# Performance work log

Hardware: AMD Instinct MI355X
Metric: run time of the kernel (lower is better)

Reference implementation:

```python
import jax, jax.numpy as jnp
import numpy as np
from jax import lax

B, T, D, A = 32, 2048, 1024, 1024

def setup_inputs() -> dict:
    key = jax.random.key(0)
    ks = jax.random.split(key, 8)
    s = 1.0 / np.sqrt(D)
    return {
        "query": jax.random.normal(ks[0], (B, 1, D), jnp.float32),
        "value": jax.random.normal(ks[1], (B, T, D), jnp.float32),
        "last_attn": jax.random.uniform(ks[2], (B, T), jnp.float32),
        "conv_w": jax.random.normal(ks[3], (A, 1, 3), jnp.float32) * 0.1,
        "conv_b": jnp.zeros((A,), jnp.float32),
        "Wq": jax.random.normal(ks[4], (A, D), jnp.float32) * s,
        "Wv": jax.random.normal(ks[5], (A, D), jnp.float32) * s,
        "bias": jax.random.uniform(ks[6], (A,), jnp.float32, -0.1, 0.1),
        "fc_w": jax.random.normal(ks[7], (1, A), jnp.float32) * (1.0 / np.sqrt(A)),
        "fc_b": jnp.zeros((1,), jnp.float32),
    }

def reference(query, value, last_attn, conv_w, conv_b, Wq, Wv, bias, fc_w, fc_b):
    # location conv1d: (B,1,T) -> (B,A,T), kernel 3, pad 1
    loc = lax.conv_general_dilated(
        last_attn[:, None, :], conv_w, window_strides=(1,), padding="SAME",
        dimension_numbers=("NCH", "OIH", "NCH"))
    loc = loc + conv_b[None, :, None]
    loc = jnp.transpose(loc, (0, 2, 1))  # (B, T, A)
    # fused add + bias + tanh; query proj (B,1,A) broadcasts over T
    hidden = jnp.tanh(query @ Wq.T + value @ Wv.T + loc + bias)  # (B, T, A)
    energy = (hidden @ fc_w.T + fc_b)[..., 0]  # (B, T)
    attn = jax.nn.softmax(energy, axis=-1)  # (B, T)
    context = jnp.einsum("bt,btd->bd", attn, value)[:, None, :]  # (B, 1, D)
    return context, attn
```

## Files before the change

kernel.cpp:

```cpp
#include <hip/hip_runtime.h>
#include <stdint.h>

#define AS1 __attribute__((address_space(1)))
#define AS3 __attribute__((address_space(3)))

typedef __bf16 bf16x8 __attribute__((ext_vector_type(8)));
typedef float  f32x4  __attribute__((ext_vector_type(4)));

__global__ __launch_bounds__(256) void cast_bf16(const float* __restrict__ in,
                                                 __bf16* __restrict__ out, int n8) {
    int i = blockIdx.x * 256 + threadIdx.x;
    if (i >= n8) return;
    const float4* p = (const float4*)in + (size_t)i * 2;
    float4 x = p[0], y = p[1];
    bf16x8 v;
    v[0] = (__bf16)x.x; v[1] = (__bf16)x.y; v[2] = (__bf16)x.z; v[3] = (__bf16)x.w;
    v[4] = (__bf16)y.x; v[5] = (__bf16)y.y; v[6] = (__bf16)y.z; v[7] = (__bf16)y.w;
    *((bf16x8*)out + i) = v;
}

__global__ __launch_bounds__(256) void prep_qb2(const float* __restrict__ q,
                                                const float* __restrict__ Wq,
                                                const float* __restrict__ bias,
                                                const float* __restrict__ convb,
                                                float* __restrict__ qb2) {
    int wid  = threadIdx.x >> 6;
    int lane = threadIdx.x & 63;
    int a    = blockIdx.x * 4 + wid;
    const float* wr_ = Wq + (size_t)a * 1024;
    float w[16];
#pragma unroll
    for (int j = 0; j < 16; ++j) w[j] = wr_[lane + 64 * j];
    float bb = bias[a] + convb[a];
    for (int b = 0; b < 32; ++b) {
        const float* qr = q + (size_t)b * 1024;
        float s = 0.f;
#pragma unroll
        for (int j = 0; j < 16; ++j) s += w[j] * qr[lane + 64 * j];
        for (int m = 1; m < 64; m <<= 1) s += __shfl_xor(s, m);
        if (lane == 0) qb2[b * 1024 + a] = s + bb;
    }
}

__global__ __launch_bounds__(256, 4) void gemm_fused(
    const __bf16* __restrict__ Abf,
    const __bf16* __restrict__ Bbf,
    const float*  __restrict__ qb2,
    const float*  __restrict__ la,
    const float*  __restrict__ convw,
    const float*  __restrict__ fcw,
    float* __restrict__ ep)
{
    constexpr int K = 1024, NT = 16;
    __shared__ __bf16 As[128 * 64];
    __shared__ __bf16 Bs[128 * 64];

    const int tid  = threadIdx.x;
    const int lane = tid & 63;
    const int wid  = tid >> 6;
    const int wr   = wid >> 1, wc = wid & 1;

    const int bid = blockIdx.x;
    const int swz = (bid & 7) * 512 + (bid >> 3);
    const int rt  = swz >> 3;
    const int ct  = swz & 7;
    const int rowBase = rt * 128;
    const int colBase = ct * 128;

    f32x4 acc[4][4] = {};

#pragma unroll 1
    for (int t = 0; t < NT; ++t) {
        const int k0 = t * 64;
#pragma unroll
        for (int is = 0; is < 4; ++is) {
            int idx16 = is * 256 + tid;
            int r     = idx16 >> 3;
            int ssw   = (idx16 ^ r) & 7;
            const __bf16* ga = Abf + (size_t)(rowBase + r) * K + k0 + ssw * 8;
            __builtin_amdgcn_global_load_lds((AS1 void*)ga, (AS3 void*)(&As[idx16 * 8]), 16, 0, 0);
            const __bf16* gb = Bbf + (size_t)(colBase + r) * K + k0 + ssw * 8;
            __builtin_amdgcn_global_load_lds((AS1 void*)gb, (AS3 void*)(&Bs[idx16 * 8]), 16, 0, 0);
        }
        __syncthreads();
#pragma unroll
        for (int kk = 0; kk < 2; ++kk) {
            bf16x8 af[4], bfr[4];
#pragma unroll
            for (int mi = 0; mi < 4; ++mi) {
                int row  = wr * 64 + mi * 16 + (lane & 15);
                int slot = (kk * 4 + (lane >> 4)) ^ (row & 7);
                af[mi] = *(const bf16x8*)(&As[row * 64 + slot * 8]);
            }
#pragma unroll
            for (int ni = 0; ni < 4; ++ni) {
                int row  = wc * 64 + ni * 16 + (lane & 15);
                int slot = (kk * 4 + (lane >> 4)) ^ (row & 7);
                bfr[ni] = *(const bf16x8*)(&Bs[row * 64 + slot * 8]);
            }
#pragma unroll
            for (int mi = 0; mi < 4; ++mi)
#pragma unroll
                for (int ni = 0; ni < 4; ++ni)
                    acc[mi][ni] = __builtin_amdgcn_mfma_f32_16x16x32_bf16(
                        af[mi], bfr[ni], acc[mi][ni], 0, 0, 0);
        }
        __syncthreads();
    }

    const int b     = rowBase >> 11;
    const int tTile = rowBase & 2047;
    const float* lab  = la  + (size_t)b * 2048;
    const float* qrow = qb2 + (size_t)b * 1024;

    float cw0[4], cw1[4], cw2[4], fv[4], qv[4];
#pragma unroll
    for (int ni = 0; ni < 4; ++ni) {
        int a = colBase + wc * 64 + ni * 16 + (lane & 15);
        cw0[ni] = convw[a * 3 + 0];
        cw1[ni] = convw[a * 3 + 1];
        cw2[ni] = convw[a * 3 + 2];
        fv[ni]  = fcw[a];
        qv[ni]  = qrow[a];
    }
    float* eps = (float*)&As[0];
    const int g4 = (lane >> 4) * 4;
#pragma unroll
    for (int mi = 0; mi < 4; ++mi) {
#pragma unroll
        for (int j = 0; j < 4; ++j) {
            int rloc = wr * 64 + mi * 16 + g4 + j;
            int t = tTile + rloc;
            float p1 = lab[t];
            float p0 = (t > 0)    ? lab[t - 1] : 0.f;
            float p2 = (t < 2047) ? lab[t + 1] : 0.f;
            float sum = 0.f;
#pragma unroll
            for (int ni = 0; ni < 4; ++ni) {
                float e = acc[mi][ni][j] + qv[ni] + cw0[ni] * p0 + cw1[ni] * p1 + cw2[ni] * p2;
                float h = 1.f - 2.f / (1.f + __expf(2.f * e));
                sum += fv[ni] * h;
            }
            sum += __shfl_xor(sum, 1);
            sum += __shfl_xor(sum, 2);
            sum += __shfl_xor(sum, 4);
            sum += __shfl_xor(sum, 8);
            if ((lane & 15) == 0)
                eps[rloc * 2 + wc] = sum;
        }
    }
    __syncthreads();
    if (tid < 128) {
        float e = eps[tid * 2 + 0] + eps[tid * 2 + 1];
        ep[(size_t)ct * 65536 + rowBase + tid] = e;
    }
}

__global__ __launch_bounds__(256) void softmax_rows(const float* __restrict__ ep,
                                                    float* __restrict__ attn) {
    int b = blockIdx.x, tid = threadIdx.x;
    float* o = attn + (size_t)b * 2048;
    __shared__ float red[4], red2[4];

    float e8[8];
#pragma unroll
    for (int k = 0; k < 8; ++k) {
        int t = tid + 256 * k;
        float s = 0.f;
#pragma unroll
        for (int ct = 0; ct < 8; ++ct) s += ep[(size_t)ct * 65536 + b * 2048 + t];
        e8[k] = s;
    }

    float m = -1e30f;
#pragma unroll
    for (int k = 0; k < 8; ++k) m = fmaxf(m, e8[k]);
    for (int s = 1; s < 64; s <<= 1) m = fmaxf(m, __shfl_xor(m, s));
    if ((tid & 63) == 0) red[tid >> 6] = m;
    __syncthreads();
    m = fmaxf(fmaxf(red[0], red[1]), fmaxf(red[2], red[3]));

    float s = 0.f, vals[8];
#pragma unroll
    for (int k = 0; k < 8; ++k) { vals[k] = __expf(e8[k] - m); s += vals[k]; }
    for (int t = 1; t < 64; t <<= 1) s += __shfl_xor(s, t);
    if ((tid & 63) == 0) red2[tid >> 6] = s;
    __syncthreads();
    s = red2[0] + red2[1] + red2[2] + red2[3];
    float inv = 1.f / s;
#pragma unroll
    for (int k = 0; k < 8; ++k) o[tid + 256 * k] = vals[k] * inv;
}

__global__ __launch_bounds__(256) void context_kernel(const float* __restrict__ attn,
                                                      const __bf16* __restrict__ vbf,
                                                      float* __restrict__ ctx) {
    int b = blockIdx.x, tc = blockIdx.y, tid = threadIdx.x;
    int half = tid >> 7, dc = tid & 127;
    const float*  ab = attn + (size_t)b * 2048 + tc * 256 + half * 128;
    const __bf16* vb = vbf + ((size_t)(b * 2048 + tc * 256 + half * 128)) * 1024 + dc * 8;
    float c[8] = {};
#pragma unroll 4
    for (int t = 0; t < 128; ++t) {
        float  w = ab[t];
        bf16x8 v = *(const bf16x8*)(vb + (size_t)t * 1024);
#pragma unroll
        for (int k = 0; k < 8; ++k) c[k] += w * (float)v[k];
    }
    float* out = ctx + (size_t)b * 1024 + dc * 8;
#pragma unroll
    for (int k = 0; k < 8; ++k) atomicAdd(out + k, c[k]);
}

extern "C" void kernel_launch(void* const* d_in, const int* in_sizes, int n_in,
                              void* d_out, int out_size, void* d_ws, size_t ws_size,
                              hipStream_t stream) {
    const float* query     = (const float*)d_in[0];
    const float* value     = (const float*)d_in[1];
    const float* last_attn = (const float*)d_in[2];
    const float* conv_w    = (const float*)d_in[3];
    const float* conv_b    = (const float*)d_in[4];
    const float* Wq        = (const float*)d_in[5];
    const float* Wv        = (const float*)d_in[6];
    const float* bias      = (const float*)d_in[7];
    const float* fc_w      = (const float*)d_in[8];

    float* ctx  = (float*)d_out;
    float* attn = (float*)d_out + 32 * 1024;

    const size_t VBF_B  = (size_t)65536 * 1024 * 2;
    const size_t WVBF_B = (size_t)1024 * 1024 * 2;
    const size_t QB2_B  = (size_t)32 * 1024 * 4;
    const size_t EP_B   = (size_t)8 * 32 * 2048 * 4;
    if (ws_size < VBF_B + WVBF_B + QB2_B + EP_B) return;

    char*   ws   = (char*)d_ws;
    __bf16* vbf  = (__bf16*)ws;
    __bf16* wvbf = (__bf16*)(ws + VBF_B);
    float*  qb2  = (float*)(ws + VBF_B + WVBF_B);
    float*  ep   = (float*)(ws + VBF_B + WVBF_B + QB2_B);

    hipMemsetAsync(ctx, 0, 32 * 1024 * sizeof(float), stream);

    cast_bf16<<<512, 256, 0, stream>>>(Wv, wvbf, 1024 * 1024 / 8);
    prep_qb2<<<256, 256, 0, stream>>>(query, Wq, bias, conv_b, qb2);
    cast_bf16<<<32768, 256, 0, stream>>>(value, vbf, 65536 * 1024 / 8);

    gemm_fused<<<4096, 256, 0, stream>>>(vbf, wvbf, qb2, last_attn, conv_w, fc_w, ep);

    softmax_rows<<<32, 256, 0, stream>>>(ep, attn);
    dim3 gc(32, 8);
    context_kernel<<<gc, 256, 0, stream>>>(attn, vbf, ctx);
}
```

Before: 307.7 us.

## Fuse prep kernels into one launch and merge softmax into context kernel

Combines the value/Wv bf16 casts, the query projection and the context zeroing into a single kernel selected by block index, replacing the memset and three launches. Softmax is merged into the context kernel: every block recomputes the row softmax from the partial energies, keeps the unnormalized weights in shared memory, and only the first column block writes attn. This removes launch gaps and a global round-trip for attn, at the cost of redundant softmax work across the 8 column blocks per row.

```diff
diff --git a/kernel.cpp b/kernel.cpp
--- a/kernel.cpp
+++ b/kernel.cpp
@@ -7,38 +7,52 @@
 typedef __bf16 bf16x8 __attribute__((ext_vector_type(8)));
 typedef float  f32x4  __attribute__((ext_vector_type(4)));
 
-__global__ __launch_bounds__(256) void cast_bf16(const float* __restrict__ in,
-                                                 __bf16* __restrict__ out, int n8) {
-    int i = blockIdx.x * 256 + threadIdx.x;
-    if (i >= n8) return;
-    const float4* p = (const float4*)in + (size_t)i * 2;
-    float4 x = p[0], y = p[1];
-    bf16x8 v;
-    v[0] = (__bf16)x.x; v[1] = (__bf16)x.y; v[2] = (__bf16)x.z; v[3] = (__bf16)x.w;
-    v[4] = (__bf16)y.x; v[5] = (__bf16)y.y; v[6] = (__bf16)y.z; v[7] = (__bf16)y.w;
-    *((bf16x8*)out + i) = v;
-}
-
-__global__ __launch_bounds__(256) void prep_qb2(const float* __restrict__ q,
-                                                const float* __restrict__ Wq,
-                                                const float* __restrict__ bias,
-                                                const float* __restrict__ convb,
-                                                float* __restrict__ qb2) {
-    int wid  = threadIdx.x >> 6;
-    int lane = threadIdx.x & 63;
-    int a    = blockIdx.x * 4 + wid;
-    const float* wr_ = Wq + (size_t)a * 1024;
-    float w[16];
-#pragma unroll
-    for (int j = 0; j < 16; ++j) w[j] = wr_[lane + 64 * j];
-    float bb = bias[a] + convb[a];
-    for (int b = 0; b < 32; ++b) {
-        const float* qr = q + (size_t)b * 1024;
-        float s = 0.f;
-#pragma unroll
-        for (int j = 0; j < 16; ++j) s += w[j] * qr[lane + 64 * j];
-        for (int m = 1; m < 64; m <<= 1) s += __shfl_xor(s, m);
-        if (lane == 0) qb2[b * 1024 + a] = s + bb;
+__global__ __launch_bounds__(256) void prep_all(
+    const float* __restrict__ value, __bf16* __restrict__ vbf,
+    const float* __restrict__ Wv,    __bf16* __restrict__ wvbf,
+    const float* __restrict__ q,     const float* __restrict__ Wq,
+    const float* __restrict__ bias,  const float* __restrict__ convb,
+    float* __restrict__ qb2,         float* __restrict__ ctx)
+{
+    const int bid = blockIdx.x, tid = threadIdx.x;
+    if (bid < 32768) {
+        int i = bid * 256 + tid;
+        const float4* p = (const float4*)value + (size_t)i * 2;
+        float4 x = p[0], y = p[1];
+        bf16x8 v;
+        v[0] = (__bf16)x.x; v[1] = (__bf16)x.y; v[2] = (__bf16)x.z; v[3] = (__bf16)x.w;
+        v[4] = (__bf16)y.x; v[5] = (__bf16)y.y; v[6] = (__bf16)y.z; v[7] = (__bf16)y.w;
+        *((bf16x8*)vbf + i) = v;
+    } else if (bid < 33280) {
+        int i = (bid - 32768) * 256 + tid;
+        const float4* p = (const float4*)Wv + (size_t)i * 2;
+        float4 x = p[0], y = p[1];
+        bf16x8 v;
+        v[0] = (__bf16)x.x; v[1] = (__bf16)x.y; v[2] = (__bf16)x.z; v[3] = (__bf16)x.w;
+        v[4] = (__bf16)y.x; v[5] = (__bf16)y.y; v[6] = (__bf16)y.z; v[7] = (__bf16)y.w;
+        *((bf16x8*)wvbf + i) = v;
+        if (i < 4096) {
+            float4 z = {0.f, 0.f, 0.f, 0.f};
+            ((float4*)ctx)[i * 2]     = z;
+            ((float4*)ctx)[i * 2 + 1] = z;
+        }
+    } else {
+        int wid  = tid >> 6;
+        int lane = tid & 63;
+        int a    = (bid - 33280) * 4 + wid;
+        const float* wr_ = Wq + (size_t)a * 1024;
+        float w[16];
+#pragma unroll
+        for (int j = 0; j < 16; ++j) w[j] = wr_[lane + 64 * j];
+        float bb = bias[a] + convb[a];
+        for (int b = 0; b < 32; ++b) {
+            const float* qr = q + (size_t)b * 1024;
+            float s = 0.f;
+#pragma unroll
+            for (int j = 0; j < 16; ++j) s += w[j] * qr[lane + 64 * j];
+            for (int m = 1; m < 64; m <<= 1) s += __shfl_xor(s, m);
+            if (lane == 0) qb2[b * 1024 + a] = s + bb;
+        }
     }
 }
 
@@ -156,13 +170,16 @@
     }
 }
 
-__global__ __launch_bounds__(256) void softmax_rows(const float* __restrict__ ep,
-                                                    float* __restrict__ attn) {
-    int b = blockIdx.x, tid = threadIdx.x;
-    float* o = attn + (size_t)b * 2048;
+__global__ __launch_bounds__(256) void context_softmax(const float* __restrict__ ep,
+                                                       const __bf16* __restrict__ vbf,
+                                                       float* __restrict__ attn,
+                                                       float* __restrict__ ctx) {
+    int b = blockIdx.x, tc = blockIdx.y, tid = threadIdx.x;
+    __shared__ float e[2048];
     __shared__ float red[4], red2[4];
 
     float e8[8];
+    float m = -1e30f;
 #pragma unroll
     for (int k = 0; k < 8; ++k) {
         int t = tid + 256 * k;
@@ -170,11 +187,8 @@
 #pragma unroll
         for (int ct = 0; ct < 8; ++ct) s += ep[(size_t)ct * 65536 + b * 2048 + t];
         e8[k] = s;
-    }
-
-    float m = -1e30f;
-#pragma unroll
-    for (int k = 0; k < 8; ++k) m = fmaxf(m, e8[k]);
+        m = fmaxf(m, s);
+    }
     for (int s = 1; s < 64; s <<= 1) m = fmaxf(m, __shfl_xor(m, s));
     if ((tid & 63) == 0) red[tid >> 6] = m;
     __syncthreads();
@@ -182,27 +196,31 @@
 
     float s = 0.f, vals[8];
 #pragma unroll
-    for (int k = 0; k < 8; ++k) { vals[k] = __expf(e8[k] - m); s += vals[k]; }
-    for (int t = 1; t < 64; t <<= 1) s += __shfl_xor(s, t);
+    for (int k = 0; k < 8; ++k) {
+        vals[k] = __expf(e8[k] - m);
+        s += vals[k];
+        e[tid + 256 * k] = vals[k];
+    }
+    for (int t2 = 1; t2 < 64; t2 <<= 1) s += __shfl_xor(s, t2);
     if ((tid & 63) == 0) red2[tid >> 6] = s;
     __syncthreads();
     s = red2[0] + red2[1] + red2[2] + red2[3];
     float inv = 1.f / s;
-#pragma unroll
-    for (int k = 0; k < 8; ++k) o[tid + 256 * k] = vals[k] * inv;
-}
-
-__global__ __launch_bounds__(256) void context_kernel(const float* __restrict__ attn,
-                                                      const __bf16* __restrict__ vbf,
-                                                      float* __restrict__ ctx) {
-    int b = blockIdx.x, tc = blockIdx.y, tid = threadIdx.x;
+
+    if (tc == 0) {
+#pragma unroll
+        for (int k = 0; k < 8; ++k)
+            attn[(size_t)b * 2048 + tid + 256 * k] = vals[k] * inv;
+    }
+
     int half = tid >> 7, dc = tid & 127;
-    const float*  ab = attn + (size_t)b * 2048 + tc * 256 + half * 128;
-    const __bf16* vb = vbf + ((size_t)(b * 2048 + tc * 256 + half * 128)) * 1024 + dc * 8;
+    int t0 = tc * 256 + half * 128;
+    const float*  wv_ = &e[t0];
+    const __bf16* vb  = vbf + ((size_t)(b * 2048 + t0)) * 1024 + dc * 8;
     float c[8] = {};
 #pragma unroll 4
     for (int t = 0; t < 128; ++t) {
-        float  w = ab[t];
+        float  w = wv_[t] * inv;
         bf16x8 v = *(const bf16x8*)(vb + (size_t)t * 1024);
 #pragma unroll
         for (int k = 0; k < 8; ++k) c[k] += w * (float)v[k];
@@ -240,15 +258,11 @@
     float*  qb2  = (float*)(ws + VBF_B + WVBF_B);
     float*  ep   = (float*)(ws + VBF_B + WVBF_B + QB2_B);
 
-    hipMemsetAsync(ctx, 0, 32 * 1024 * sizeof(float), stream);
-
-    cast_bf16<<<512, 256, 0, stream>>>(Wv, wvbf, 1024 * 1024 / 8);
-    prep_qb2<<<256, 256, 0, stream>>>(query, Wq, bias, conv_b, qb2);
-    cast_bf16<<<32768, 256, 0, stream>>>(value, vbf, 65536 * 1024 / 8);
+    prep_all<<<33536, 256, 0, stream>>>(value, vbf, Wv, wvbf,
+                                        query, Wq, bias, conv_b, qb2, ctx);
 
     gemm_fused<<<4096, 256, 0, stream>>>(vbf, wvbf, qb2, last_attn, conv_w, fc_w, ep);
 
-    softmax_rows<<<32, 256, 0, stream>>>(ep, attn);
     dim3 gc(32, 8);
-    context_kernel<<<gc, 256, 0, stream>>>(attn, vbf, ctx);
-}
+    context_softmax<<<gc, 256, 0, stream>>>(ep, vbf, attn, ctx);
+}
```

Result: faster. 296.6 us, median of 3 (-3.6%).
